# Optimization experiments

Hardware: AMD Instinct MI355X
Metric: run time of the kernel (lower is better)

Reference implementation:

```python
import jax, jax.numpy as jnp
import numpy as np

B, G = 128, 20000
HID = 64
NUM_BINS = 10
LEAKY_SLOPE = 0.01  # torch nn.LeakyReLU default


def setup_inputs() -> dict:
    key = jax.random.key(0)
    k1, k2, k3, k4, k5, k6 = jax.random.split(key, 6)
    vals = jax.random.normal(k1, (B, G), dtype=jnp.float32)
    keep = jax.random.uniform(k2, (B, G)) < 0.1
    expr_value = jnp.where(keep, vals, 0.0)
    # MLP params: Linear(1 -> HID), Linear(HID -> NUM_BINS-1)
    W1 = jax.random.normal(k3, (1, HID), dtype=jnp.float32) * 0.5
    b1 = jax.random.normal(k4, (HID,), dtype=jnp.float32) * 0.1
    W2 = jax.random.normal(k5, (HID, NUM_BINS - 1), dtype=jnp.float32) * (1.0 / np.sqrt(HID))
    b2 = jax.random.normal(k6, (NUM_BINS - 1,), dtype=jnp.float32) * 0.1
    return {"expr_value": expr_value, "W1": W1, "b1": b1, "W2": W2, "b2": b2}


def reference(expr_value, W1, b1, W2, b2):
    # mask of nonzero expression positions (B, G)
    mask_expr = (expr_value != 0).astype(jnp.float32)
    # tiny MLP applied to every position (vectorized; zero positions masked out below)
    x = expr_value[..., None]                      # (B, G, 1)
    h = x * W1[0] + b1                             # (B, G, HID); Linear(1->HID)
    h = jnp.where(h >= 0, h, LEAKY_SLOPE * h)      # LeakyReLU
    logits = jnp.einsum('bgh,hk->bgk', h, W2) + b2 # (B, G, NUM_BINS-1)
    p = jax.nn.softmax(logits, axis=-1)            # softmax over bins 1..num_bins-1
    m = mask_expr[..., None]
    # bin 0 prob = 1 where expr==0 else 0; bins 1.. = softmax where expr!=0 else 0
    probs = jnp.concatenate([1.0 - m, p * m], axis=-1)  # (B, G, NUM_BINS)
    return probs, mask_expr
```

## Files before the change

kernel.cpp:

```cpp
#include <hip/hip_runtime.h>
#include <math.h>

#define HID 64
#define KB 9
#define NB 10
#define NTOT (128 * 20000)
#define BLOCK 256
#define EPB 2048
#define FEPT 2
#define LEAKY 0.01f
#define RSTRIDE 20
#define SENT 3.0e38f
#define LOG2E 1.44269504088896f

#define NBUK 2048
#define BLO (-6.0f)
#define BSCALE (2048.0f / 12.0f)

#define TAB_U32 (128 + 65 * RSTRIDE)
#define WS_U32 (TAB_U32 + NBUK / 4)
#define WS_BYTES (WS_U32 * 4)

typedef float v4f __attribute__((ext_vector_type(4)));
typedef float v2f __attribute__((ext_vector_type(2)));

__global__ __launch_bounds__(64) void setup_kernel(
    const float* __restrict__ W1, const float* __restrict__ b1,
    const float* __restrict__ W2, const float* __restrict__ b2,
    float* __restrict__ ws)
{
    __shared__ float t_lds[HID], w_lds[HID], b_lds[HID], tsrt[HID];
    __shared__ float w2_lds[HID * KB];
    __shared__ float red[18 * 65];

    const int j = threadIdx.x;
    const int blk = blockIdx.x;
    const float w = W1[j], b = b1[j];
    const float t = (w != 0.0f) ? (-b / w) : -SENT;
    t_lds[j] = t; w_lds[j] = w; b_lds[j] = b;
    if (blk < 65) {
        #pragma unroll
        for (int q = j; q < HID * KB; q += 64) w2_lds[q] = W2[q];
    }
    __syncthreads();

    int rank = 0;
    for (int i = 0; i < HID; ++i) {
        float ti = t_lds[i];
        rank += (ti < t || (ti == t && i < j)) ? 1 : 0;
    }
    tsrt[rank] = t;
    __syncthreads();

    if (blk >= 65) {
        const int bb = (blk - 65) * 64 + j;
        const float edge = BLO + ((float)bb - 0.5f) * (1.0f / BSCALE);
        int cnt = 0;
        for (int i = 0; i < HID; ++i) cnt += (tsrt[i] <= edge) ? 1 : 0;
        ((unsigned char*)(ws + TAB_U32))[bb] = (bb == 0) ? 0 : (unsigned char)cnt;
        return;
    }

    const int r = blk;
    float xm;
    if (r == 0)        xm = tsrt[0] - 1.0f;
    else if (r == HID) xm = tsrt[HID - 1] + 1.0f;
    else               xm = 0.5f * (tsrt[r - 1] + tsrt[r]);

    const float s = (fmaf(w, xm, b) >= 0.0f) ? 1.0f : LEAKY;
    #pragma unroll
    for (int k = 0; k < KB; ++k) {
        const float w2s = w2_lds[j * KB + k] * s;
        red[(2 * k) * 65 + j]     = w2s * w;
        red[(2 * k + 1) * 65 + j] = w2s * b;
    }
    __syncthreads();

    if (j < 18) {
        float acc = 0.0f;
        for (int i = 0; i < HID; ++i) acc += red[j * 65 + i];
        const int k = j >> 1;
        if (j & 1) ws[128 + r * RSTRIDE + KB + k] = (acc + b2[k]) * LOG2E;
        else       ws[128 + r * RSTRIDE + k]      = acc * LOG2E;
    }
    if (r == 0) { ws[j] = tsrt[j]; ws[64 + j] = SENT; }
}

__global__ __launch_bounds__(BLOCK) void main_kernel(
    const float* __restrict__ expr, const float* __restrict__ ws,
    float* __restrict__ out)
{
    __shared__ __align__(16) unsigned int sdata[WS_U32];
    __shared__ float xs[EPB];
    __shared__ unsigned short list[EPB];
    __shared__ int swsum[4];

    const int tid = threadIdx.x;
    const int lane = tid & 63, wv = tid >> 6;

    #pragma unroll
    for (int t = tid; t < WS_U32 / 4; t += BLOCK)
        ((v4f*)sdata)[t] = ((const v4f*)ws)[t];

    const size_t e0 = (size_t)blockIdx.x * EPB;
    const v4f xa = ((const v4f*)(expr + e0))[tid];
    const v4f xb = ((const v4f*)(expr + e0))[BLOCK + tid];
    ((v4f*)xs)[tid] = xa;
    ((v4f*)xs)[BLOCK + tid] = xb;
    const float xr[8] = {xa.x, xa.y, xa.z, xa.w, xb.x, xb.y, xb.z, xb.w};

    int c = 0;
    #pragma unroll
    for (int j = 0; j < 8; ++j) c += (xr[j] != 0.0f) ? 1 : 0;

    int incl = c;
    #pragma unroll
    for (int d = 1; d < 64; d <<= 1) {
        int n = __shfl_up(incl, d, 64);
        if (lane >= d) incl += n;
    }
    if (lane == 63) swsum[wv] = incl;
    __syncthreads();

    const int s0 = swsum[0], s1 = swsum[1], s2 = swsum[2], s3 = swsum[3];
    const int total = s0 + s1 + s2 + s3;
    int base = (incl - c) + (wv > 0 ? s0 : 0) + (wv > 1 ? s1 : 0) + (wv > 2 ? s2 : 0);

    #pragma unroll
    for (int j = 0; j < 8; ++j) {
        if (xr[j] != 0.0f) {
            const int eidx = (j < 4) ? (4 * tid + j) : (1024 + 4 * tid + (j - 4));
            list[base++] = (unsigned short)eidx;
        }
    }

    float* mout = out + (size_t)NTOT * NB + e0;
    const v4f ma = {xr[0] != 0.f ? 1.f : 0.f, xr[1] != 0.f ? 1.f : 0.f,
                    xr[2] != 0.f ? 1.f : 0.f, xr[3] != 0.f ? 1.f : 0.f};
    const v4f mb = {xr[4] != 0.f ? 1.f : 0.f, xr[5] != 0.f ? 1.f : 0.f,
                    xr[6] != 0.f ? 1.f : 0.f, xr[7] != 0.f ? 1.f : 0.f};
    ((v4f*)mout)[tid] = ma;
    ((v4f*)mout)[BLOCK + tid] = mb;

    float* gout = out + e0 * NB;
    #pragma unroll
    for (int q = 0; q < 20; ++q) {
        const int g = q * BLOCK + tid;
        const int r5 = g % 5;
        const v4f v = {r5 == 0 ? 1.0f : 0.0f, 0.0f, r5 == 2 ? 1.0f : 0.0f, 0.0f};
        ((v4f*)gout)[g] = v;
    }

    __syncthreads();

    const float* ts  = (const float*)sdata;
    const float* tab = (const float*)sdata + 128;
    const unsigned char* buk = (const unsigned char*)(sdata + TAB_U32);

    for (int i = tid; i < total; i += BLOCK) {
        const int e = list[i];
        const float xe = xs[e];
        const float fb = fminf(2047.0f, fmaxf(0.0f, (xe - BLO) * BSCALE));
        int idx = buk[(int)fb];
        while (ts[idx] <= xe) ++idx;
        const v4f* rowv = (const v4f*)(tab + idx * RSTRIDE);
        const v4f r0 = rowv[0], r1 = rowv[1], r2 = rowv[2], r3 = rowv[3], r4 = rowv[4];
        const float A[KB] = {r0.x, r0.y, r0.z, r0.w, r1.x, r1.y, r1.z, r1.w, r2.x};
        const float C[KB] = {r2.y, r2.z, r2.w, r3.x, r3.y, r3.z, r3.w, r4.x, r4.y};
        float lg[KB];
        #pragma unroll
        for (int k = 0; k < KB; ++k) lg[k] = fmaf(A[k], xe, C[k]);
        float m = lg[0];
        #pragma unroll
        for (int k = 1; k < KB; ++k) m = fmaxf(m, lg[k]);
        float p[KB];
        float s = 0.0f;
        #pragma unroll
        for (int k = 0; k < KB; ++k) { p[k] = exp2f(lg[k] - m); s += p[k]; }
        const float rcp = __frcp_rn(s);
        v2f* po = (v2f*)(gout + (size_t)e * NB);
        po[0] = (v2f){0.0f,        p[0] * rcp};
        po[1] = (v2f){p[1] * rcp,  p[2] * rcp};
        po[2] = (v2f){p[3] * rcp,  p[4] * rcp};
        po[3] = (v2f){p[5] * rcp,  p[6] * rcp};
        po[4] = (v2f){p[7] * rcp,  p[8] * rcp};
    }
}

__global__ __launch_bounds__(BLOCK) void fused_kernel(
    const float* __restrict__ expr,
    const float* __restrict__ W1, const float* __restrict__ b1,
    const float* __restrict__ W2, const float* __restrict__ b2,
    float* __restrict__ out)
{
    __shared__ float ts[128];
    __shared__ float tab[65 * RSTRIDE];
    __shared__ float st[HID], sw[HID], sb[HID], tsrt[HID];
    const int tid = threadIdx.x;
    if (tid < HID) {
        float w = W1[tid], b = b1[tid];
        st[tid] = (w != 0.0f) ? (-b / w) : -SENT;
        sw[tid] = w; sb[tid] = b;
    }
    __syncthreads();
    if (tid < HID) {
        float t = st[tid];
        int r = 0;
        for (int i = 0; i < HID; ++i) {
            float ti = st[i];
            r += (ti < t || (ti == t && i < tid)) ? 1 : 0;
        }
        tsrt[r] = t;
    }
    __syncthreads();
    if (tid < 128) ts[tid] = (tid < HID) ? tsrt[tid] : SENT;
    for (int item = tid; item < 65 * KB; item += BLOCK) {
        int r = item / KB, k = item - r * KB;
        float xm;
        if (r == 0)        xm = tsrt[0] - 1.0f;
        else if (r == HID) xm = tsrt[HID - 1] + 1.0f;
        else               xm = 0.5f * (tsrt[r - 1] + tsrt[r]);
        float A = 0.0f, C = b2[k];
        for (int j = 0; j < HID; ++j) {
            float w = sw[j], bb = sb[j];
            float s = (fmaf(w, xm, bb) >= 0.0f) ? 1.0f : LEAKY;
            float w2s = W2[j * KB + k] * s;
            A = fmaf(w2s, w, A);
            C = fmaf(w2s, bb, C);
        }
        tab[r * RSTRIDE + k] = A;
        tab[r * RSTRIDE + KB + k] = C;
    }
    __syncthreads();
    const int i0 = (blockIdx.x * BLOCK + tid) * FEPT;
    const float2 xv = *(const float2*)(expr + i0);
    float x[FEPT] = {xv.x, xv.y};
    float o[FEPT * NB]; float msk[FEPT];
    #pragma unroll
    for (int e = 0; e < FEPT; ++e) {
        const float xe = x[e];
        int idx = 0;
        #pragma unroll
        for (int s = 64; s >= 1; s >>= 1) idx += (ts[idx + s - 1] <= xe) ? s : 0;
        const float* row = tab + idx * RSTRIDE;
        float lg[KB];
        #pragma unroll
        for (int k = 0; k < KB; ++k) lg[k] = fmaf(row[k], xe, row[KB + k]);
        float m = lg[0];
        #pragma unroll
        for (int k = 1; k < KB; ++k) m = fmaxf(m, lg[k]);
        float p[KB]; float s = 0.0f;
        #pragma unroll
        for (int k = 0; k < KB; ++k) { p[k] = __expf(lg[k] - m); s += p[k]; }
        const float rcp = __frcp_rn(s);
        const bool nz = (xe != 0.0f);
        msk[e] = nz ? 1.0f : 0.0f;
        o[e * NB] = nz ? 0.0f : 1.0f;
        #pragma unroll
        for (int k = 0; k < KB; ++k) o[e * NB + 1 + k] = nz ? p[k] * rcp : 0.0f;
    }
    float* dst = out + (size_t)i0 * NB;
    #pragma unroll
    for (int q = 0; q < FEPT * NB / 4; ++q) ((float4*)dst)[q] = ((const float4*)o)[q];
    *(float2*)(out + (size_t)NTOT * NB + i0) = make_float2(msk[0], msk[1]);
}

extern "C" void kernel_launch(void* const* d_in, const int* in_sizes, int n_in,
                              void* d_out, int out_size, void* d_ws, size_t ws_size,
                              hipStream_t stream) {
    const float* expr = (const float*)d_in[0];
    const float* W1   = (const float*)d_in[1];
    const float* b1   = (const float*)d_in[2];
    const float* W2   = (const float*)d_in[3];
    const float* b2   = (const float*)d_in[4];
    float* out = (float*)d_out;

    if (ws_size >= (size_t)WS_BYTES) {
        float* ws = (float*)d_ws;
        setup_kernel<<<65 + NBUK / 64, 64, 0, stream>>>(W1, b1, W2, b2, ws);
        main_kernel<<<NTOT / EPB, BLOCK, 0, stream>>>(expr, ws, out);
    } else {
        fused_kernel<<<NTOT / (BLOCK * FEPT), BLOCK, 0, stream>>>(expr, W1, b1, W2, b2, out);
    }
}
```

Before: 135.9 us.

## Stage probability rows in LDS tiles and write output with coalesced nontemporal stores

Instead of first writing default zero/one rows to global memory and then scattering 40-byte rows for nonzero entries, the kernel computes softmax rows into a shared-memory tile per 512-element chunk. It then writes full coalesced v4 nontemporal stores that merge the defaults with the computed rows. This removes the double write of the output and the uncoalesced scattered stores. Element-to-thread mapping is changed to contiguous 8 per thread so the compacted list stays sorted, and chunk boundaries are found by binary search. The cost is extra LDS use, more barriers per chunk and some divide/select arithmetic per store.

```diff
diff --git a/kernel.cpp b/kernel.cpp
--- a/kernel.cpp
+++ b/kernel.cpp
@@ -7,6 +7,8 @@
 #define NTOT (128 * 20000)
 #define BLOCK 256
 #define EPB 2048
+#define CHUNK 512
+#define NCHUNK (EPB / CHUNK)
 #define FEPT 2
 #define LEAKY 0.01f
 #define RSTRIDE 20
@@ -91,9 +93,11 @@
     float* __restrict__ out)
 {
     __shared__ __align__(16) unsigned int sdata[WS_U32];
-    __shared__ float xs[EPB];
+    __shared__ __align__(16) float xs[EPB];
+    __shared__ __align__(16) float tile[CHUNK * NB];
     __shared__ unsigned short list[EPB];
     __shared__ int swsum[4];
+    __shared__ int bnd[NCHUNK];
 
     const int tid = threadIdx.x;
     const int lane = tid & 63, wv = tid >> 6;
@@ -103,87 +107,117 @@
         ((v4f*)sdata)[t] = ((const v4f*)ws)[t];
 
     const size_t e0 = (size_t)blockIdx.x * EPB;
-    const v4f xa = ((const v4f*)(expr + e0))[tid];
-    const v4f xb = ((const v4f*)(expr + e0))[BLOCK + tid];
-    ((v4f*)xs)[tid] = xa;
-    ((v4f*)xs)[BLOCK + tid] = xb;
+    const v4f xa = ((const v4f*)(expr + e0))[2 * tid];
+    const v4f xb = ((const v4f*)(expr + e0))[2 * tid + 1];
+    ((v4f*)xs)[2 * tid] = xa;
+    ((v4f*)xs)[2 * tid + 1] = xb;
     const float xr[8] = {xa.x, xa.y, xa.z, xa.w, xb.x, xb.y, xb.z, xb.w};
 
-    int c = 0;
-    #pragma unroll
-    for (int j = 0; j < 8; ++j) c += (xr[j] != 0.0f) ? 1 : 0;
-
-    int incl = c;
+    int cnt = 0;
+    #pragma unroll
+    for (int j = 0; j < 8; ++j) cnt += (xr[j] != 0.0f) ? 1 : 0;
+
+    int incl = cnt;
     #pragma unroll
     for (int d = 1; d < 64; d <<= 1) {
         int n = __shfl_up(incl, d, 64);
         if (lane >= d) incl += n;
     }
     if (lane == 63) swsum[wv] = incl;
-    __syncthreads();
-
-    const int s0 = swsum[0], s1 = swsum[1], s2 = swsum[2], s3 = swsum[3];
-    const int total = s0 + s1 + s2 + s3;
-    int base = (incl - c) + (wv > 0 ? s0 : 0) + (wv > 1 ? s1 : 0) + (wv > 2 ? s2 : 0);
-
-    #pragma unroll
-    for (int j = 0; j < 8; ++j) {
-        if (xr[j] != 0.0f) {
-            const int eidx = (j < 4) ? (4 * tid + j) : (1024 + 4 * tid + (j - 4));
-            list[base++] = (unsigned short)eidx;
-        }
-    }
 
     float* mout = out + (size_t)NTOT * NB + e0;
     const v4f ma = {xr[0] != 0.f ? 1.f : 0.f, xr[1] != 0.f ? 1.f : 0.f,
                     xr[2] != 0.f ? 1.f : 0.f, xr[3] != 0.f ? 1.f : 0.f};
     const v4f mb = {xr[4] != 0.f ? 1.f : 0.f, xr[5] != 0.f ? 1.f : 0.f,
                     xr[6] != 0.f ? 1.f : 0.f, xr[7] != 0.f ? 1.f : 0.f};
-    ((v4f*)mout)[tid] = ma;
-    ((v4f*)mout)[BLOCK + tid] = mb;
-
-    float* gout = out + e0 * NB;
-    #pragma unroll
-    for (int q = 0; q < 20; ++q) {
-        const int g = q * BLOCK + tid;
-        const int r5 = g % 5;
-        const v4f v = {r5 == 0 ? 1.0f : 0.0f, 0.0f, r5 == 2 ? 1.0f : 0.0f, 0.0f};
-        ((v4f*)gout)[g] = v;
-    }
-
+    __builtin_nontemporal_store(ma, ((v4f*)mout) + 2 * tid);
+    __builtin_nontemporal_store(mb, ((v4f*)mout) + 2 * tid + 1);
+
+    __syncthreads();
+
+    const int s0 = swsum[0], s1 = swsum[1], s2 = swsum[2], s3 = swsum[3];
+    const int total = s0 + s1 + s2 + s3;
+    int base = (incl - cnt) + (wv > 0 ? s0 : 0) + (wv > 1 ? s1 : 0) + (wv > 2 ? s2 : 0);
+
+    #pragma unroll
+    for (int j = 0; j < 8; ++j) {
+        if (xr[j] != 0.0f) list[base++] = (unsigned short)(8 * tid + j);
+    }
+
+    __syncthreads();
+
+    if (tid < NCHUNK - 1) {
+        const int target = (tid + 1) * CHUNK;
+        int lo = 0, hi = total;
+        while (lo < hi) {
+            const int mid = (lo + hi) >> 1;
+            if ((int)list[mid] < target) lo = mid + 1; else hi = mid;
+        }
+        bnd[tid + 1] = lo;
+    }
     __syncthreads();
 
     const float* ts  = (const float*)sdata;
     const float* tab = (const float*)sdata + 128;
     const unsigned char* buk = (const unsigned char*)(sdata + TAB_U32);
-
-    for (int i = tid; i < total; i += BLOCK) {
-        const int e = list[i];
-        const float xe = xs[e];
-        const float fb = fminf(2047.0f, fmaxf(0.0f, (xe - BLO) * BSCALE));
-        int idx = buk[(int)fb];
-        while (ts[idx] <= xe) ++idx;
-        const v4f* rowv = (const v4f*)(tab + idx * RSTRIDE);
-        const v4f r0 = rowv[0], r1 = rowv[1], r2 = rowv[2], r3 = rowv[3], r4 = rowv[4];
-        const float A[KB] = {r0.x, r0.y, r0.z, r0.w, r1.x, r1.y, r1.z, r1.w, r2.x};
-        const float C[KB] = {r2.y, r2.z, r2.w, r3.x, r3.y, r3.z, r3.w, r4.x, r4.y};
-        float lg[KB];
-        #pragma unroll
-        for (int k = 0; k < KB; ++k) lg[k] = fmaf(A[k], xe, C[k]);
-        float m = lg[0];
-        #pragma unroll
-        for (int k = 1; k < KB; ++k) m = fmaxf(m, lg[k]);
-        float p[KB];
-        float s = 0.0f;
-        #pragma unroll
-        for (int k = 0; k < KB; ++k) { p[k] = exp2f(lg[k] - m); s += p[k]; }
-        const float rcp = __frcp_rn(s);
-        v2f* po = (v2f*)(gout + (size_t)e * NB);
-        po[0] = (v2f){0.0f,        p[0] * rcp};
-        po[1] = (v2f){p[1] * rcp,  p[2] * rcp};
-        po[2] = (v2f){p[3] * rcp,  p[4] * rcp};
-        po[3] = (v2f){p[5] * rcp,  p[6] * rcp};
-        po[4] = (v2f){p[7] * rcp,  p[8] * rcp};
+    float* gout = out + e0 * NB;
+
+    for (int ch = 0; ch < NCHUNK; ++ch) {
+        const int lo = (ch == 0) ? 0 : bnd[ch];
+        const int hi = (ch == NCHUNK - 1) ? total : bnd[ch + 1];
+
+        for (int i = lo + tid; i < hi; i += BLOCK) {
+            const int e = list[i];
+            const float xe = xs[e];
+            const float fb = fminf(2047.0f, fmaxf(0.0f, (xe - BLO) * BSCALE));
+            int idx = buk[(int)fb];
+            while (ts[idx] <= xe) ++idx;
+            const v4f* rowv = (const v4f*)(tab + idx * RSTRIDE);
+            const v4f r0 = rowv[0], r1 = rowv[1], r2 = rowv[2], r3 = rowv[3], r4 = rowv[4];
+            const float A[KB] = {r0.x, r0.y, r0.z, r0.w, r1.x, r1.y, r1.z, r1.w, r2.x};
+            const float C[KB] = {r2.y, r2.z, r2.w, r3.x, r3.y, r3.z, r3.w, r4.x, r4.y};
+            float lg[KB];
+            #pragma unroll
+            for (int k = 0; k < KB; ++k) lg[k] = fmaf(A[k], xe, C[k]);
+            float m = lg[0];
+            #pragma unroll
+            for (int k = 1; k < KB; ++k) m = fmaxf(m, lg[k]);
+            float p[KB];
+            float s = 0.0f;
+            #pragma unroll
+            for (int k = 0; k < KB; ++k) { p[k] = exp2f(lg[k] - m); s += p[k]; }
+            const float rcp = __frcp_rn(s);
+            v2f* po = (v2f*)(tile + (e - ch * CHUNK) * NB);
+            po[0] = (v2f){0.0f,        p[0] * rcp};
+            po[1] = (v2f){p[1] * rcp,  p[2] * rcp};
+            po[2] = (v2f){p[3] * rcp,  p[4] * rcp};
+            po[3] = (v2f){p[5] * rcp,  p[6] * rcp};
+            po[4] = (v2f){p[7] * rcp,  p[8] * rcp};
+        }
+        __syncthreads();
+
+        const int cb = ch * CHUNK;
+        #pragma unroll
+        for (int q = 0; q < (CHUNK * NB) / (4 * BLOCK); ++q) {
+            const int g = q * BLOCK + tid;
+            const unsigned p0 = 4u * (unsigned)g;
+            const unsigned ea = p0 / 10u;
+            const int rb = (int)(p0 - 10u * ea);
+            const int ebi = ((int)ea + 1 < CHUNK) ? (int)ea + 1 : CHUNK - 1;
+            const float xva = xs[cb + (int)ea];
+            const float xvb = xs[cb + ebi];
+            const v4f tv = ((const v4f*)tile)[g];
+            v4f res;
+            #pragma unroll
+            for (int j = 0; j < 4; ++j) {
+                const int t = rb + j;
+                const float xv = (t >= 10) ? xvb : xva;
+                const float dfl = (t == 0 || t == 10) ? 1.0f : 0.0f;
+                res[j] = (xv != 0.0f) ? tv[j] : dfl;
+            }
+            __builtin_nontemporal_store(res, ((v4f*)gout) + (ch * (CHUNK * NB / 4) + g));
+        }
+        __syncthreads();
     }
 }
 
```

New measurement: 142.5 us. +4.8%, slower.
